# Performance work log

Hardware: AMD Instinct MI355X
Metric: run time of the kernel (lower is better)

Reference implementation:

```python
import jax, jax.numpy as jnp
import numpy as np
from math import sqrt

B, S, E = 1, 2048, 1024
H, D = 16, 1024          # num_heads, d_model
DH = D // H              # head_dim = 64
EPS = 1e-5
LAMBDA_INIT = 0.8


def setup_inputs() -> dict:
    key = jax.random.key(0)
    ks = jax.random.split(key, 16)
    sd = 0.02
    x = jax.random.normal(ks[0], (B, S, E), dtype=jnp.float32)
    # causal mask: True => masked (matches torch masked_fill semantics)
    mask = jnp.triu(jnp.ones((S, S), dtype=bool), k=1)
    # per-head projection params stacked over heads: W [H, DH, E], b [H, DH]
    mk = lambda k: jax.random.normal(k, (H, DH, E), dtype=jnp.float32) * sd
    bk = lambda k: jax.random.normal(k, (H, DH), dtype=jnp.float32) * sd
    return {
        "x": x, "mask": mask,
        "Wq1": mk(ks[1]), "bq1": bk(ks[2]),
        "Wq2": mk(ks[3]), "bq2": bk(ks[4]),
        "Wk1": mk(ks[5]), "bk1": bk(ks[6]),
        "Wk2": mk(ks[7]), "bk2": bk(ks[8]),
        "Wv": mk(ks[9]), "bv": bk(ks[10]),
        "lam": jnp.full((H,), LAMBDA_INIT, dtype=jnp.float32),
        "gn_w": jnp.ones((D,), dtype=jnp.float32),
        "gn_b": jnp.zeros((D,), dtype=jnp.float32),
        "Wo": jax.random.normal(ks[11], (E, D), dtype=jnp.float32) * sd,
        "bo": jax.random.normal(ks[12], (E,), dtype=jnp.float32) * sd,
    }


def reference(x, mask, Wq1, bq1, Wq2, bq2, Wk1, bk1, Wk2, bk2, Wv, bv,
              lam, gn_w, gn_b, Wo, bo):
    scale = 1.0 / sqrt(DH)
    proj = lambda W, b: jnp.einsum('bse,hde->bhsd', x, W) + b[None, :, None, :]
    q1, q2 = proj(Wq1, bq1), proj(Wq2, bq2)
    k1, k2 = proj(Wk1, bk1), proj(Wk2, bk2)
    v = proj(Wv, bv)                                   # [B,H,S,DH]

    neg_inf = jnp.float32(-jnp.inf)
    s1 = jnp.einsum('bhsd,bhtd->bhst', q1, k1) * scale  # [B,H,S,S]
    s2 = jnp.einsum('bhsd,bhtd->bhst', q2, k2) * scale
    s1 = jnp.where(mask, neg_inf, s1)
    s2 = jnp.where(mask, neg_inf, s2)
    w = jax.nn.softmax(s1, axis=-1) - lam[None, :, None, None] * jax.nn.softmax(s2, axis=-1)
    # dropout is identity in eval mode
    out = jnp.einsum('bhst,bhtd->bhsd', w, v)           # [B,H,S,DH]

    # concat heads along feature dim -> [B,S,D]
    cat = out.transpose(0, 2, 1, 3).reshape(B, S, D)
    # GroupNorm over channels with num_groups=H: normalize each (DH, S) group
    xc = cat.transpose(0, 2, 1).reshape(B, H, DH, S)    # [B,H,DH,S]
    mu = xc.mean(axis=(2, 3), keepdims=True)
    var = xc.var(axis=(2, 3), keepdims=True)
    xn = ((xc - mu) * jax.lax.rsqrt(var + EPS)).reshape(B, D, S)
    xn = xn * gn_w[None, :, None] + gn_b[None, :, None]
    xn = xn.transpose(0, 2, 1)                          # [B,S,D]

    return xn @ Wo.T + bo                               # [B,S,E]
```

## Files before the change

kernel.cpp:

```cpp
#include <hip/hip_runtime.h>

#define S_LEN 2048
#define E_DIM 1024
#define NH 16
#define DHD 64
#define DMODEL 1024

typedef unsigned short u16;
typedef __attribute__((ext_vector_type(8))) short bf16x8;
typedef __attribute__((ext_vector_type(4))) float f32x4;

static constexpr float GN_EPS = 1e-5f;
static constexpr float QSCALE_LOG2E = 0.125f * 1.44269504088896340736f;

struct alignas(8) U16x4 { u16 x, y, z, w; };

__device__ __forceinline__ u16 f2bf(float f) {
    union { float f; unsigned u; } v; v.f = f;
    unsigned r = v.u + 0x7fffu + ((v.u >> 16) & 1u);
    return (u16)(r >> 16);
}

__device__ __forceinline__ f32x4 fzero() { f32x4 z = {0.f, 0.f, 0.f, 0.f}; return z; }

__device__ __forceinline__ void async16(const u16* g, u16* l) {
    __builtin_amdgcn_global_load_lds(
        (const __attribute__((address_space(1))) unsigned int*)g,
        (__attribute__((address_space(3))) unsigned int*)l, 16, 0, 0);
}

__device__ __forceinline__ void stage8(const u16* gbase, int gstride, u16* lds,
                                       int r0, int l) {
    const int cg = (l & 7) ^ (l >> 3);
    async16(gbase + (size_t)(r0 + (l >> 3)) * gstride + cg * 8, lds + r0 * 64);
}

__device__ __forceinline__ bf16x8 ldsfrag(const u16* lds, int r, int chunk) {
    return *(const bf16x8*)((const char*)lds + r * 128 + ((chunk ^ (r & 7)) << 4));
}

__global__ __launch_bounds__(256) void f2b_kernel(
    const float* __restrict__ x,
    const float* __restrict__ w0, const float* __restrict__ w1,
    const float* __restrict__ w2, const float* __restrict__ w3,
    const float* __restrict__ w4, const float* __restrict__ wo,
    u16* __restrict__ xb, u16* __restrict__ wall, u16* __restrict__ dwo)
{
    const int z = blockIdx.z;
    const float* src; u16* dst; int n;
    const int nw = NH * DHD * E_DIM;
    switch (z) {
        case 0: src = x;  dst = xb;            n = S_LEN * E_DIM;  break;
        case 1: src = w0; dst = wall;          n = nw; break;
        case 2: src = w1; dst = wall + nw;     n = nw; break;
        case 3: src = w2; dst = wall + 2 * nw; n = nw; break;
        case 4: src = w3; dst = wall + 3 * nw; n = nw; break;
        case 5: src = w4; dst = wall + 4 * nw; n = nw; break;
        default: src = wo; dst = dwo;          n = DMODEL * E_DIM; break;
    }
    int i = blockIdx.x * 256 + threadIdx.x;
    if (i * 4 < n) {
        float4 v = ((const float4*)src)[i];
        U16x4 o;
        o.x = f2bf(v.x); o.y = f2bf(v.y); o.z = f2bf(v.z); o.w = f2bf(v.w);
        ((U16x4*)dst)[i] = o;
    }
}

__global__ __launch_bounds__(256) void proj_mfma_kernel(
    const u16* __restrict__ xb, const u16* __restrict__ wall,
    const float* __restrict__ bq1, const float* __restrict__ bq2,
    const float* __restrict__ bk1, const float* __restrict__ bk2,
    const float* __restrict__ bv,
    u16* __restrict__ qk, u16* __restrict__ vt)
{
    __shared__ u16 As[128 * 64], Bs[128 * 64];
    const int m0 = blockIdx.x * 128, n0 = blockIdx.y * 128;
    const int t = threadIdx.x, w = t >> 6, l = t & 63;
    const int lane15 = l & 15, quad = l >> 4;
    const int wr = (w >> 1) * 64, wc = (w & 1) * 64;

    f32x4 acc[4][4];
    #pragma unroll
    for (int mi = 0; mi < 4; ++mi)
        #pragma unroll
        for (int ni = 0; ni < 4; ++ni) acc[mi][ni] = fzero();

    const u16* Ag = xb + (size_t)m0 * E_DIM;
    const u16* Bg = wall + (size_t)n0 * E_DIM;

    for (int k0 = 0; k0 < E_DIM; k0 += 64) {
        __syncthreads();
        #pragma unroll
        for (int i = 0; i < 4; ++i) stage8(Ag + k0, E_DIM, As, w * 32 + i * 8, l);
        #pragma unroll
        for (int i = 0; i < 4; ++i) stage8(Bg + k0, E_DIM, Bs, w * 32 + i * 8, l);
        __syncthreads();

        bf16x8 a[4][2], b[4][2];
        #pragma unroll
        for (int mi = 0; mi < 4; ++mi) {
            a[mi][0] = ldsfrag(As, wr + mi * 16 + lane15, quad);
            a[mi][1] = ldsfrag(As, wr + mi * 16 + lane15, 4 + quad);
        }
        #pragma unroll
        for (int ni = 0; ni < 4; ++ni) {
            b[ni][0] = ldsfrag(Bs, wc + ni * 16 + lane15, quad);
            b[ni][1] = ldsfrag(Bs, wc + ni * 16 + lane15, 4 + quad);
        }
        #pragma unroll
        for (int mi = 0; mi < 4; ++mi)
            #pragma unroll
            for (int ni = 0; ni < 4; ++ni) {
                acc[mi][ni] = __builtin_amdgcn_mfma_f32_16x16x32_bf16(
                    a[mi][0], b[ni][0], acc[mi][ni], 0, 0, 0);
                acc[mi][ni] = __builtin_amdgcn_mfma_f32_16x16x32_bf16(
                    a[mi][1], b[ni][1], acc[mi][ni], 0, 0, 0);
            }
    }

    const int tid = n0 >> 10;
    const float* bias = (tid == 0) ? bq1 : (tid == 1) ? bq2 :
                        (tid == 2) ? bk1 : (tid == 3) ? bk2 : bv;
    const float scl = (tid <= 1) ? QSCALE_LOG2E : 1.0f;
    const size_t nQKV = (size_t)NH * S_LEN * DHD;

    #pragma unroll
    for (int ni = 0; ni < 4; ++ni) {
        const int n = n0 + wc + ni * 16 + lane15;
        const int h = (n >> 6) & 15, d = n & 63;
        const float bb = bias[n & 1023];
        #pragma unroll
        for (int mi = 0; mi < 4; ++mi) {
            const int m = m0 + wr + mi * 16 + quad * 4;
            if (tid < 4) {
                u16* o = qk + tid * nQKV + ((size_t)h * S_LEN + m) * DHD + d;
                #pragma unroll
                for (int r = 0; r < 4; ++r)
                    o[r * DHD] = f2bf((acc[mi][ni][r] + bb) * scl);
            } else {
                U16x4 pk;
                pk.x = f2bf(acc[mi][ni][0] + bb);
                pk.y = f2bf(acc[mi][ni][1] + bb);
                pk.z = f2bf(acc[mi][ni][2] + bb);
                pk.w = f2bf(acc[mi][ni][3] + bb);
                *(U16x4*)(vt + ((size_t)h * DHD + d) * S_LEN + m) = pk;
            }
        }
    }
}

__global__ __launch_bounds__(256) void attn_mfma_kernel(
    const u16* __restrict__ qbase, const u16* __restrict__ kbase,
    const u16* __restrict__ vtb, float* __restrict__ obase)
{
    __shared__ u16 Qs[64 * 64];
    __shared__ u16 Ks[2][64 * 64], Vs[2][64 * 64];
    __shared__ u16 Ps[4][16 * 64];
    const int z = blockIdx.z, h = blockIdx.y, bb = blockIdx.x;
    const size_t per = (size_t)NH * S_LEN * DHD;
    const u16* qg = qbase + z * per + (size_t)h * S_LEN * DHD;
    const u16* kg = kbase + z * per + (size_t)h * S_LEN * DHD;
    const u16* vg = vtb + (size_t)h * DHD * S_LEN;
    float* og = obase + z * per + (size_t)h * S_LEN * DHD;
    const int t = threadIdx.x, w = t >> 6, l = t & 63;
    const int lane15 = l & 15, quad = l >> 4;
    u16* Pw = Ps[w];

    for (int half = 0; half < 2; ++half) {
        const int qt = half ? (31 - bb) : bb;
        const int q0 = qt * 64;
        stage8(qg + (size_t)q0 * DHD, DHD, Qs, w * 16, l);
        stage8(qg + (size_t)q0 * DHD, DHD, Qs, w * 16 + 8, l);
        stage8(kg, DHD, Ks[0], w * 16, l);
        stage8(kg, DHD, Ks[0], w * 16 + 8, l);
        stage8(vg, S_LEN, Vs[0], w * 16, l);
        stage8(vg, S_LEN, Vs[0], w * 16 + 8, l);

        f32x4 O[4];
        float lsum[4];
        #pragma unroll
        for (int i = 0; i < 4; ++i) { O[i] = fzero(); lsum[i] = 0.f; }
        bf16x8 qa0, qa1;

        for (int kt = 0; kt <= qt; ++kt) {
            const int cur = kt & 1;
            __syncthreads();
            if (kt < qt) {
                const int t1 = (kt + 1) * 64;
                stage8(kg + (size_t)t1 * DHD, DHD, Ks[cur ^ 1], w * 16, l);
                stage8(kg + (size_t)t1 * DHD, DHD, Ks[cur ^ 1], w * 16 + 8, l);
                stage8(vg + t1, S_LEN, Vs[cur ^ 1], w * 16, l);
                stage8(vg + t1, S_LEN, Vs[cur ^ 1], w * 16 + 8, l);
            }
            if (kt == 0) {
                qa0 = ldsfrag(Qs, w * 16 + lane15, quad);
                qa1 = ldsfrag(Qs, w * 16 + lane15, 4 + quad);
            }

            f32x4 sc[4];
            #pragma unroll
            for (int nt = 0; nt < 4; ++nt) {
                sc[nt] = fzero();
                bf16x8 b0 = ldsfrag(Ks[cur], nt * 16 + lane15, quad);
                bf16x8 b1 = ldsfrag(Ks[cur], nt * 16 + lane15, 4 + quad);
                sc[nt] = __builtin_amdgcn_mfma_f32_16x16x32_bf16(qa0, b0, sc[nt], 0, 0, 0);
                sc[nt] = __builtin_amdgcn_mfma_f32_16x16x32_bf16(qa1, b1, sc[nt], 0, 0, 0);
            }

            const bool diag = (kt == qt);
            #pragma unroll
            for (int r = 0; r < 4; ++r) {
                const int lr = quad * 4 + r;
                const int qrl = w * 16 + lr;
                float p0 = __builtin_amdgcn_exp2f(sc[0][r]);
                float p1 = __builtin_amdgcn_exp2f(sc[1][r]);
                float p2 = __builtin_amdgcn_exp2f(sc[2][r]);
                float p3 = __builtin_amdgcn_exp2f(sc[3][r]);
                if (diag) {
                    if (lane15      > qrl) p0 = 0.f;
                    if (16 + lane15 > qrl) p1 = 0.f;
                    if (32 + lane15 > qrl) p2 = 0.f;
                    if (48 + lane15 > qrl) p3 = 0.f;
                }
                lsum[r] += (p0 + p1) + (p2 + p3);
                const int cb = (lane15 & 7) * 2;
                const int ch = lane15 >> 3;
                char* pb = (char*)Pw + lr * 128;
                *(u16*)(pb + (((0 + ch) ^ (lr & 7)) << 4) + cb) = f2bf(p0);
                *(u16*)(pb + (((2 + ch) ^ (lr & 7)) << 4) + cb) = f2bf(p1);
                *(u16*)(pb + (((4 + ch) ^ (lr & 7)) << 4) + cb) = f2bf(p2);
                *(u16*)(pb + (((6 + ch) ^ (lr & 7)) << 4) + cb) = f2bf(p3);
            }

            bf16x8 pa0 = ldsfrag(Pw, lane15, quad);
            bf16x8 pa1 = ldsfrag(Pw, lane15, 4 + quad);
            #pragma unroll
            for (int nt = 0; nt < 4; ++nt) {
                bf16x8 v0 = ldsfrag(Vs[cur], nt * 16 + lane15, quad);
                bf16x8 v1 = ldsfrag(Vs[cur], nt * 16 + lane15, 4 + quad);
                O[nt] = __builtin_amdgcn_mfma_f32_16x16x32_bf16(pa0, v0, O[nt], 0, 0, 0);
                O[nt] = __builtin_amdgcn_mfma_f32_16x16x32_bf16(pa1, v1, O[nt], 0, 0, 0);
            }
        }

        float inv[4];
        #pragma unroll
        for (int r = 0; r < 4; ++r) {
            float rs = lsum[r];
            rs += __shfl_xor(rs, 1);
            rs += __shfl_xor(rs, 2);
            rs += __shfl_xor(rs, 4);
            rs += __shfl_xor(rs, 8);
            inv[r] = 1.f / rs;
        }
        float* orow = og + (size_t)(q0 + w * 16 + quad * 4) * DHD;
        #pragma unroll
        for (int nt = 0; nt < 4; ++nt) {
            const int d = nt * 16 + lane15;
            #pragma unroll
            for (int r = 0; r < 4; ++r)
                orow[r * DHD + d] = O[nt][r] * inv[r];
        }
        __syncthreads();
    }
}

__global__ __launch_bounds__(256) void gn_stats_kernel(
    const float* __restrict__ o1, const float* __restrict__ o2,
    const float* __restrict__ lam, float* __restrict__ part)
{
    const int h = blockIdx.x, p = blockIdx.y;
    const float vlam = lam[h];
    const int chunk = S_LEN * DHD / 8;
    const size_t base = (size_t)h * (S_LEN * DHD) + (size_t)p * chunk;
    const float4* a = (const float4*)(o1 + base);
    const float4* b = (const float4*)(o2 + base);
    float s = 0.f, ss = 0.f;
    for (int i = threadIdx.x; i < chunk / 4; i += 256) {
        float4 av = a[i], bv = b[i];
        float v0 = av.x - vlam * bv.x;
        float v1 = av.y - vlam * bv.y;
        float v2 = av.z - vlam * bv.z;
        float v3 = av.w - vlam * bv.w;
        s  += (v0 + v1) + (v2 + v3);
        ss += (v0 * v0 + v1 * v1) + (v2 * v2 + v3 * v3);
    }
    #pragma unroll
    for (int d = 1; d < 64; d <<= 1) { s += __shfl_xor(s, d); ss += __shfl_xor(ss, d); }
    __shared__ float red[8];
    const int w = threadIdx.x >> 6;
    if ((threadIdx.x & 63) == 0) { red[2 * w] = s; red[2 * w + 1] = ss; }
    __syncthreads();
    if (threadIdx.x == 0) {
        float S  = (red[0] + red[2]) + (red[4] + red[6]);
        float SS = (red[1] + red[3]) + (red[5] + red[7]);
        part[(blockIdx.x * 8 + p) * 2]     = S;
        part[(blockIdx.x * 8 + p) * 2 + 1] = SS;
    }
}

__global__ __launch_bounds__(256) void gn_apply_kernel(
    const float* __restrict__ o1, const float* __restrict__ o2,
    const float* __restrict__ lam, const float* __restrict__ part,
    const float* __restrict__ gw, const float* __restrict__ gb,
    u16* __restrict__ xnb)
{
    int i = blockIdx.x * 256 + threadIdx.x;
    int dh = i & 63;
    int s  = (i >> 6) & (S_LEN - 1);
    int h  = i >> 17;
    int d  = h * DHD + dh;
    float sum = 0.f, ssum = 0.f;
    #pragma unroll
    for (int p = 0; p < 8; ++p) {
        sum  += part[(h * 8 + p) * 2];
        ssum += part[(h * 8 + p) * 2 + 1];
    }
    const float n = (float)(S_LEN * DHD);
    const float mu = sum / n;
    const float rstd = rsqrtf(ssum / n - mu * mu + GN_EPS);
    float v = o1[i] - lam[h] * o2[i];
    xnb[(size_t)s * DMODEL + d] = f2bf((v - mu) * rstd * gw[d] + gb[d]);
}

__global__ __launch_bounds__(256) void out_mfma_kernel(
    const u16* __restrict__ xnb, const u16* __restrict__ wob,
    const float* __restrict__ bo, float* __restrict__ out)
{
    __shared__ u16 As[64 * 64], Bs[64 * 64];
    const int m0 = blockIdx.x * 64, n0 = blockIdx.y * 64;
    const int t = threadIdx.x, w = t >> 6, l = t & 63;
    const int lane15 = l & 15, quad = l >> 4;
    f32x4 acc[4];
    #pragma unroll
    for (int nt = 0; nt < 4; ++nt) acc[nt] = fzero();

    const u16* Ag = xnb + (size_t)m0 * DMODEL;
    const u16* Bg = wob + (size_t)n0 * DMODEL;
    for (int k0 = 0; k0 < DMODEL; k0 += 64) {
        __syncthreads();
        stage8(Ag + k0, DMODEL, As, w * 16, l);
        stage8(Ag + k0, DMODEL, As, w * 16 + 8, l);
        stage8(Bg + k0, DMODEL, Bs, w * 16, l);
        stage8(Bg + k0, DMODEL, Bs, w * 16 + 8, l);
        __syncthreads();
        bf16x8 a0 = ldsfrag(As, w * 16 + lane15, quad);
        bf16x8 a1 = ldsfrag(As, w * 16 + lane15, 4 + quad);
        #pragma unroll
        for (int nt = 0; nt < 4; ++nt) {
            bf16x8 b0 = ldsfrag(Bs, nt * 16 + lane15, quad);
            bf16x8 b1 = ldsfrag(Bs, nt * 16 + lane15, 4 + quad);
            acc[nt] = __builtin_amdgcn_mfma_f32_16x16x32_bf16(a0, b0, acc[nt], 0, 0, 0);
            acc[nt] = __builtin_amdgcn_mfma_f32_16x16x32_bf16(a1, b1, acc[nt], 0, 0, 0);
        }
    }
    #pragma unroll
    for (int nt = 0; nt < 4; ++nt) {
        const int n = n0 + nt * 16 + lane15;
        const float bb = bo[n];
        #pragma unroll
        for (int r = 0; r < 4; ++r)
            out[(size_t)(m0 + w * 16 + quad * 4 + r) * E_DIM + n] = acc[nt][r] + bb;
    }
}

extern "C" void kernel_launch(void* const* d_in, const int* in_sizes, int n_in,
                              void* d_out, int out_size, void* d_ws, size_t ws_size,
                              hipStream_t stream)
{
    const float* x   = (const float*)d_in[0];
    const float* Wq1 = (const float*)d_in[2];
    const float* bq1 = (const float*)d_in[3];
    const float* Wq2 = (const float*)d_in[4];
    const float* bq2 = (const float*)d_in[5];
    const float* Wk1 = (const float*)d_in[6];
    const float* bk1 = (const float*)d_in[7];
    const float* Wk2 = (const float*)d_in[8];
    const float* bk2 = (const float*)d_in[9];
    const float* Wv  = (const float*)d_in[10];
    const float* bv  = (const float*)d_in[11];
    const float* lam = (const float*)d_in[12];
    const float* gw  = (const float*)d_in[13];
    const float* gb  = (const float*)d_in[14];
    const float* Wo  = (const float*)d_in[15];
    const float* bo  = (const float*)d_in[16];
    float* out = (float*)d_out;

    char* p = (char*)d_ws;
    auto take = [&](size_t bytes) { char* r = p; p += (bytes + 255) & ~(size_t)255; return r; };
    const size_t nQKV = (size_t)NH * S_LEN * DHD;

    u16* xb   = (u16*)take(2 * (size_t)S_LEN * E_DIM);
    u16* wall = (u16*)take(2 * (size_t)5 * NH * DHD * E_DIM);
    u16* wob  = (u16*)take(2 * (size_t)DMODEL * E_DIM);
    u16* qk   = (u16*)take(2 * 4 * nQKV);
    u16* vtb  = (u16*)take(2 * nQKV);
    float* o1 = (float*)take(4 * 2 * nQKV);
    u16* xnb  = (u16*)take(2 * (size_t)S_LEN * DMODEL);
    float* part = (float*)take(4 * 256);

    f2b_kernel<<<dim3(2048, 1, 7), 256, 0, stream>>>(
        x, Wq1, Wq2, Wk1, Wk2, Wv, Wo, xb, wall, wob);

    proj_mfma_kernel<<<dim3(16, 40), 256, 0, stream>>>(
        xb, wall, bq1, bq2, bk1, bk2, bv, qk, vtb);

    attn_mfma_kernel<<<dim3(16, NH, 2), 256, 0, stream>>>(
        qk, qk + 2 * nQKV, vtb, o1);

    gn_stats_kernel<<<dim3(NH, 8), 256, 0, stream>>>(o1, o1 + nQKV, lam, part);
    gn_apply_kernel<<<dim3((int)(nQKV / 256)), 256, 0, stream>>>(
        o1, o1 + nQKV, lam, part, gw, gb, xnb);

    out_mfma_kernel<<<dim3(32, 16), 256, 0, stream>>>(xnb, wob, bo, out);
}
```

Measured before the change: 226.6 us.

## Store attention outputs as bf16, split attention into one q-tile per block, vectorize groupnorm

The attention kernel now processes one query tile per block, scheduled longest-first, instead of pairing tiles bb and 31-bb in one block. This doubles the grid and is meant to improve occupancy and load balance. Attention outputs are written as bf16 rather than fp32, which halves the traffic that the group-norm stats and apply kernels read. Those kernels are vectorized to unpack packed bf16, and P is truncated to bf16 instead of rounded. The cost is lower precision in the intermediate outputs and in P, plus losing the paired-tile balancing inside each block.

```diff
diff --git a/kernel.cpp b/kernel.cpp
--- a/kernel.cpp
+++ b/kernel.cpp
@@ -19,6 +19,13 @@
     union { float f; unsigned u; } v; v.f = f;
     unsigned r = v.u + 0x7fffu + ((v.u >> 16) & 1u);
     return (u16)(r >> 16);
+}
+__device__ __forceinline__ u16 f2bf_trunc(float f) {
+    union { float f; unsigned u; } v; v.f = f;
+    return (u16)(v.u >> 16);
+}
+__device__ __forceinline__ float bf2f(u16 u) {
+    union { unsigned u; float f; } v; v.u = ((unsigned)u) << 16; return v.f;
 }
 
 __device__ __forceinline__ f32x4 fzero() { f32x4 z = {0.f, 0.f, 0.f, 0.f}; return z; }
@@ -152,139 +159,142 @@
 
 __global__ __launch_bounds__(256) void attn_mfma_kernel(
     const u16* __restrict__ qbase, const u16* __restrict__ kbase,
-    const u16* __restrict__ vtb, float* __restrict__ obase)
+    const u16* __restrict__ vtb, u16* __restrict__ obase)
 {
     __shared__ u16 Qs[64 * 64];
     __shared__ u16 Ks[2][64 * 64], Vs[2][64 * 64];
     __shared__ u16 Ps[4][16 * 64];
-    const int z = blockIdx.z, h = blockIdx.y, bb = blockIdx.x;
+    const int z = blockIdx.z, h = blockIdx.y;
+    const int qt = 31 - blockIdx.x;
+    const int q0 = qt * 64;
     const size_t per = (size_t)NH * S_LEN * DHD;
     const u16* qg = qbase + z * per + (size_t)h * S_LEN * DHD;
     const u16* kg = kbase + z * per + (size_t)h * S_LEN * DHD;
     const u16* vg = vtb + (size_t)h * DHD * S_LEN;
-    float* og = obase + z * per + (size_t)h * S_LEN * DHD;
+    u16* og = obase + z * per + (size_t)h * S_LEN * DHD;
     const int t = threadIdx.x, w = t >> 6, l = t & 63;
     const int lane15 = l & 15, quad = l >> 4;
     u16* Pw = Ps[w];
 
-    for (int half = 0; half < 2; ++half) {
-        const int qt = half ? (31 - bb) : bb;
-        const int q0 = qt * 64;
-        stage8(qg + (size_t)q0 * DHD, DHD, Qs, w * 16, l);
-        stage8(qg + (size_t)q0 * DHD, DHD, Qs, w * 16 + 8, l);
-        stage8(kg, DHD, Ks[0], w * 16, l);
-        stage8(kg, DHD, Ks[0], w * 16 + 8, l);
-        stage8(vg, S_LEN, Vs[0], w * 16, l);
-        stage8(vg, S_LEN, Vs[0], w * 16 + 8, l);
-
-        f32x4 O[4];
-        float lsum[4];
-        #pragma unroll
-        for (int i = 0; i < 4; ++i) { O[i] = fzero(); lsum[i] = 0.f; }
-        bf16x8 qa0, qa1;
-
-        for (int kt = 0; kt <= qt; ++kt) {
-            const int cur = kt & 1;
-            __syncthreads();
-            if (kt < qt) {
-                const int t1 = (kt + 1) * 64;
-                stage8(kg + (size_t)t1 * DHD, DHD, Ks[cur ^ 1], w * 16, l);
-                stage8(kg + (size_t)t1 * DHD, DHD, Ks[cur ^ 1], w * 16 + 8, l);
-                stage8(vg + t1, S_LEN, Vs[cur ^ 1], w * 16, l);
-                stage8(vg + t1, S_LEN, Vs[cur ^ 1], w * 16 + 8, l);
+    stage8(qg + (size_t)q0 * DHD, DHD, Qs, w * 16, l);
+    stage8(qg + (size_t)q0 * DHD, DHD, Qs, w * 16 + 8, l);
+    stage8(kg, DHD, Ks[0], w * 16, l);
+    stage8(kg, DHD, Ks[0], w * 16 + 8, l);
+    stage8(vg, S_LEN, Vs[0], w * 16, l);
+    stage8(vg, S_LEN, Vs[0], w * 16 + 8, l);
+
+    f32x4 O[4];
+    float lsum[4];
+    #pragma unroll
+    for (int i = 0; i < 4; ++i) { O[i] = fzero(); lsum[i] = 0.f; }
+    bf16x8 qa0, qa1;
+
+    for (int kt = 0; kt <= qt; ++kt) {
+        const int cur = kt & 1;
+        __syncthreads();
+        if (kt < qt) {
+            const int t1 = (kt + 1) * 64;
+            stage8(kg + (size_t)t1 * DHD, DHD, Ks[cur ^ 1], w * 16, l);
+            stage8(kg + (size_t)t1 * DHD, DHD, Ks[cur ^ 1], w * 16 + 8, l);
+            stage8(vg + t1, S_LEN, Vs[cur ^ 1], w * 16, l);
+            stage8(vg + t1, S_LEN, Vs[cur ^ 1], w * 16 + 8, l);
+        }
+        if (kt == 0) {
+            qa0 = ldsfrag(Qs, w * 16 + lane15, quad);
+            qa1 = ldsfrag(Qs, w * 16 + lane15, 4 + quad);
+        }
+
+        f32x4 sc[4];
+        #pragma unroll
+        for (int nt = 0; nt < 4; ++nt) {
+            sc[nt] = fzero();
+            bf16x8 b0 = ldsfrag(Ks[cur], nt * 16 + lane15, quad);
+            bf16x8 b1 = ldsfrag(Ks[cur], nt * 16 + lane15, 4 + quad);
+            sc[nt] = __builtin_amdgcn_mfma_f32_16x16x32_bf16(qa0, b0, sc[nt], 0, 0, 0);
+            sc[nt] = __builtin_amdgcn_mfma_f32_16x16x32_bf16(qa1, b1, sc[nt], 0, 0, 0);
+        }
+
+        const bool diag = (kt == qt);
+        #pragma unroll
+        for (int r = 0; r < 4; ++r) {
+            const int lr = quad * 4 + r;
+            const int qrl = w * 16 + lr;
+            float p0 = __builtin_amdgcn_exp2f(sc[0][r]);
+            float p1 = __builtin_amdgcn_exp2f(sc[1][r]);
+            float p2 = __builtin_amdgcn_exp2f(sc[2][r]);
+            float p3 = __builtin_amdgcn_exp2f(sc[3][r]);
+            if (diag) {
+                if (lane15      > qrl) p0 = 0.f;
+                if (16 + lane15 > qrl) p1 = 0.f;
+                if (32 + lane15 > qrl) p2 = 0.f;
+                if (48 + lane15 > qrl) p3 = 0.f;
             }
-            if (kt == 0) {
-                qa0 = ldsfrag(Qs, w * 16 + lane15, quad);
-                qa1 = ldsfrag(Qs, w * 16 + lane15, 4 + quad);
-            }
-
-            f32x4 sc[4];
-            #pragma unroll
-            for (int nt = 0; nt < 4; ++nt) {
-                sc[nt] = fzero();
-                bf16x8 b0 = ldsfrag(Ks[cur], nt * 16 + lane15, quad);
-                bf16x8 b1 = ldsfrag(Ks[cur], nt * 16 + lane15, 4 + quad);
-                sc[nt] = __builtin_amdgcn_mfma_f32_16x16x32_bf16(qa0, b0, sc[nt], 0, 0, 0);
-                sc[nt] = __builtin_amdgcn_mfma_f32_16x16x32_bf16(qa1, b1, sc[nt], 0, 0, 0);
-            }
-
-            const bool diag = (kt == qt);
-            #pragma unroll
-            for (int r = 0; r < 4; ++r) {
-                const int lr = quad * 4 + r;
-                const int qrl = w * 16 + lr;
-                float p0 = __builtin_amdgcn_exp2f(sc[0][r]);
-                float p1 = __builtin_amdgcn_exp2f(sc[1][r]);
-                float p2 = __builtin_amdgcn_exp2f(sc[2][r]);
-                float p3 = __builtin_amdgcn_exp2f(sc[3][r]);
-                if (diag) {
-                    if (lane15      > qrl) p0 = 0.f;
-                    if (16 + lane15 > qrl) p1 = 0.f;
-                    if (32 + lane15 > qrl) p2 = 0.f;
-                    if (48 + lane15 > qrl) p3 = 0.f;
-                }
-                lsum[r] += (p0 + p1) + (p2 + p3);
-                const int cb = (lane15 & 7) * 2;
-                const int ch = lane15 >> 3;
-                char* pb = (char*)Pw + lr * 128;
-                *(u16*)(pb + (((0 + ch) ^ (lr & 7)) << 4) + cb) = f2bf(p0);
-                *(u16*)(pb + (((2 + ch) ^ (lr & 7)) << 4) + cb) = f2bf(p1);
-                *(u16*)(pb + (((4 + ch) ^ (lr & 7)) << 4) + cb) = f2bf(p2);
-                *(u16*)(pb + (((6 + ch) ^ (lr & 7)) << 4) + cb) = f2bf(p3);
-            }
-
-            bf16x8 pa0 = ldsfrag(Pw, lane15, quad);
-            bf16x8 pa1 = ldsfrag(Pw, lane15, 4 + quad);
-            #pragma unroll
-            for (int nt = 0; nt < 4; ++nt) {
-                bf16x8 v0 = ldsfrag(Vs[cur], nt * 16 + lane15, quad);
-                bf16x8 v1 = ldsfrag(Vs[cur], nt * 16 + lane15, 4 + quad);
-                O[nt] = __builtin_amdgcn_mfma_f32_16x16x32_bf16(pa0, v0, O[nt], 0, 0, 0);
-                O[nt] = __builtin_amdgcn_mfma_f32_16x16x32_bf16(pa1, v1, O[nt], 0, 0, 0);
-            }
-        }
-
-        float inv[4];
-        #pragma unroll
-        for (int r = 0; r < 4; ++r) {
-            float rs = lsum[r];
-            rs += __shfl_xor(rs, 1);
-            rs += __shfl_xor(rs, 2);
-            rs += __shfl_xor(rs, 4);
-            rs += __shfl_xor(rs, 8);
-            inv[r] = 1.f / rs;
-        }
-        float* orow = og + (size_t)(q0 + w * 16 + quad * 4) * DHD;
+            lsum[r] += (p0 + p1) + (p2 + p3);
+            const int cb = (lane15 & 7) * 2;
+            const int ch = lane15 >> 3;
+            char* pb = (char*)Pw + lr * 128;
+            *(u16*)(pb + (((0 + ch) ^ (lr & 7)) << 4) + cb) = f2bf_trunc(p0);
+            *(u16*)(pb + (((2 + ch) ^ (lr & 7)) << 4) + cb) = f2bf_trunc(p1);
+            *(u16*)(pb + (((4 + ch) ^ (lr & 7)) << 4) + cb) = f2bf_trunc(p2);
+            *(u16*)(pb + (((6 + ch) ^ (lr & 7)) << 4) + cb) = f2bf_trunc(p3);
+        }
+
+        bf16x8 pa0 = ldsfrag(Pw, lane15, quad);
+        bf16x8 pa1 = ldsfrag(Pw, lane15, 4 + quad);
         #pragma unroll
         for (int nt = 0; nt < 4; ++nt) {
-            const int d = nt * 16 + lane15;
-            #pragma unroll
-            for (int r = 0; r < 4; ++r)
-                orow[r * DHD + d] = O[nt][r] * inv[r];
-        }
-        __syncthreads();
+            bf16x8 v0 = ldsfrag(Vs[cur], nt * 16 + lane15, quad);
+            bf16x8 v1 = ldsfrag(Vs[cur], nt * 16 + lane15, 4 + quad);
+            O[nt] = __builtin_amdgcn_mfma_f32_16x16x32_bf16(pa0, v0, O[nt], 0, 0, 0);
+            O[nt] = __builtin_amdgcn_mfma_f32_16x16x32_bf16(pa1, v1, O[nt], 0, 0, 0);
+        }
+    }
+
+    float inv[4];
+    #pragma unroll
+    for (int r = 0; r < 4; ++r) {
+        float rs = lsum[r];
+        rs += __shfl_xor(rs, 1);
+        rs += __shfl_xor(rs, 2);
+        rs += __shfl_xor(rs, 4);
+        rs += __shfl_xor(rs, 8);
+        inv[r] = 1.f / rs;
+    }
+    u16* orow = og + (size_t)(q0 + w * 16 + quad * 4) * DHD;
+    #pragma unroll
+    for (int nt = 0; nt < 4; ++nt) {
+        const int d = nt * 16 + lane15;
+        #pragma unroll
+        for (int r = 0; r < 4; ++r)
+            orow[r * DHD + d] = f2bf(O[nt][r] * inv[r]);
     }
 }
 
 __global__ __launch_bounds__(256) void gn_stats_kernel(
-    const float* __restrict__ o1, const float* __restrict__ o2,
+    const u16* __restrict__ o1, const u16* __restrict__ o2,
     const float* __restrict__ lam, float* __restrict__ part)
 {
     const int h = blockIdx.x, p = blockIdx.y;
     const float vlam = lam[h];
     const int chunk = S_LEN * DHD / 8;
     const size_t base = (size_t)h * (S_LEN * DHD) + (size_t)p * chunk;
-    const float4* a = (const float4*)(o1 + base);
-    const float4* b = (const float4*)(o2 + base);
+    const uint4* a = (const uint4*)(o1 + base);
+    const uint4* b = (const uint4*)(o2 + base);
     float s = 0.f, ss = 0.f;
-    for (int i = threadIdx.x; i < chunk / 4; i += 256) {
-        float4 av = a[i], bv = b[i];
-        float v0 = av.x - vlam * bv.x;
-        float v1 = av.y - vlam * bv.y;
-        float v2 = av.z - vlam * bv.z;
-        float v3 = av.w - vlam * bv.w;
-        s  += (v0 + v1) + (v2 + v3);
-        ss += (v0 * v0 + v1 * v1) + (v2 * v2 + v3 * v3);
+    for (int i = threadIdx.x; i < chunk / 8; i += 256) {
+        uint4 av = a[i], bv = b[i];
+        const unsigned aw[4] = {av.x, av.y, av.z, av.w};
+        const unsigned bw[4] = {bv.x, bv.y, bv.z, bv.w};
+        #pragma unroll
+        for (int j = 0; j < 4; ++j) {
+            union { unsigned u; float f; } lo_a, hi_a, lo_b, hi_b;
+            lo_a.u = aw[j] << 16; hi_a.u = aw[j] & 0xffff0000u;
+            lo_b.u = bw[j] << 16; hi_b.u = bw[j] & 0xffff0000u;
+            float v0 = lo_a.f - vlam * lo_b.f;
+            float v1 = hi_a.f - vlam * hi_b.f;
+            s += v0 + v1;
+            ss += v0 * v0 + v1 * v1;
+        }
     }
     #pragma unroll
     for (int d = 1; d < 64; d <<= 1) { s += __shfl_xor(s, d); ss += __shfl_xor(ss, d); }
@@ -301,16 +311,16 @@
 }
 
 __global__ __launch_bounds__(256) void gn_apply_kernel(
-    const float* __restrict__ o1, const float* __restrict__ o2,
+    const u16* __restrict__ o1, const u16* __restrict__ o2,
     const float* __restrict__ lam, const float* __restrict__ part,
     const float* __restrict__ gw, const float* __restrict__ gb,
     u16* __restrict__ xnb)
 {
-    int i = blockIdx.x * 256 + threadIdx.x;
-    int dh = i & 63;
-    int s  = (i >> 6) & (S_LEN - 1);
-    int h  = i >> 17;
-    int d  = h * DHD + dh;
+    const int i4 = (blockIdx.x * 256 + threadIdx.x) * 4;
+    const int dh = i4 & 63;
+    const int s  = (i4 >> 6) & (S_LEN - 1);
+    const int h  = i4 >> 17;
+    const int d  = h * DHD + dh;
     float sum = 0.f, ssum = 0.f;
     #pragma unroll
     for (int p = 0; p < 8; ++p) {
@@ -320,8 +330,17 @@
     const float n = (float)(S_LEN * DHD);
     const float mu = sum / n;
     const float rstd = rsqrtf(ssum / n - mu * mu + GN_EPS);
-    float v = o1[i] - lam[h] * o2[i];
-    xnb[(size_t)s * DMODEL + d] = f2bf((v - mu) * rstd * gw[d] + gb[d]);
+    const float vlam = lam[h];
+    U16x4 a = *(const U16x4*)(o1 + i4);
+    U16x4 b = *(const U16x4*)(o2 + i4);
+    float4 g4 = *(const float4*)(gw + d);
+    float4 b4 = *(const float4*)(gb + d);
+    U16x4 o;
+    o.x = f2bf((bf2f(a.x) - vlam * bf2f(b.x) - mu) * rstd * g4.x + b4.x);
+    o.y = f2bf((bf2f(a.y) - vlam * bf2f(b.y) - mu) * rstd * g4.y + b4.y);
+    o.z = f2bf((bf2f(a.z) - vlam * bf2f(b.z) - mu) * rstd * g4.z + b4.z);
+    o.w = f2bf((bf2f(a.w) - vlam * bf2f(b.w) - mu) * rstd * g4.w + b4.w);
+    *(U16x4*)(xnb + (size_t)s * DMODEL + d) = o;
 }
 
 __global__ __launch_bounds__(256) void out_mfma_kernel(
@@ -396,7 +415,7 @@
     u16* wob  = (u16*)take(2 * (size_t)DMODEL * E_DIM);
     u16* qk   = (u16*)take(2 * 4 * nQKV);
     u16* vtb  = (u16*)take(2 * nQKV);
-    float* o1 = (float*)take(4 * 2 * nQKV);
+    u16* o1   = (u16*)take(2 * 2 * nQKV);
     u16* xnb  = (u16*)take(2 * (size_t)S_LEN * DMODEL);
     float* part = (float*)take(4 * 256);
 
@@ -406,11 +425,11 @@
     proj_mfma_kernel<<<dim3(16, 40), 256, 0, stream>>>(
         xb, wall, bq1, bq2, bk1, bk2, bv, qk, vtb);
 
-    attn_mfma_kernel<<<dim3(16, NH, 2), 256, 0, stream>>>(
+    attn_mfma_kernel<<<dim3(32, NH, 2), 256, 0, stream>>>(
         qk, qk + 2 * nQKV, vtb, o1);
 
     gn_stats_kernel<<<dim3(NH, 8), 256, 0, stream>>>(o1, o1 + nQKV, lam, part);
-    gn_apply_kernel<<<dim3((int)(nQKV / 256)), 256, 0, stream>>>(
+    gn_apply_kernel<<<dim3((int)(nQKV / 1024)), 256, 0, stream>>>(
         o1, o1 + nQKV, lam, part, gw, gb, xnb);
 
     out_mfma_kernel<<<dim3(32, 16), 256, 0, stream>>>(xnb, wob, bo, out);
```

Measured after the change: 249.7 us. 1.1x slower.
